# Optimization experiments

Hardware: AMD Instinct MI355X
Metric: run time of the kernel (lower is better)

## Reference

```python
import jax, jax.numpy as jnp
import numpy as np

SLOPE = 0.2  # LeakyReLU slope (DGCNN convention)

def _conv1x1(x, W, b):
    # x: [B, N, Cin], W: [Cout, Cin] -> [B, N, Cout] (Conv2d 1x1 == shared MLP)
    return jnp.einsum('bnc,oc->bno', x, W) + b

def _edgeconv(x, k, Wa, ba, Wb, bb):
    # DGCNN EdgeConv: kNN in feature space, edge MLP on (x_j - x_i, x_i), max-aggregate.
    # x: [B, N, C]
    sq = jnp.sum(x * x, axis=-1)                       # [B, N]
    inner = jnp.einsum('bnc,bmc->bnm', x, x)           # [B, N, N]
    dist = sq[:, :, None] - 2.0 * inner + sq[:, None, :]
    _, idx = jax.lax.top_k(-dist, k)                   # [B, N, k] (includes self)
    nb = jax.vmap(lambda xb, ib: xb[ib])(x, idx)       # [B, N, k, C] gather neighbors
    xi = jnp.broadcast_to(x[:, :, None, :], nb.shape)
    e = jnp.concatenate([nb - xi, xi], axis=-1)        # [B, N, k, 2C]
    h = jax.nn.leaky_relu(jnp.einsum('bnke,oe->bnko', e, Wa) + ba, SLOPE)
    h = jax.nn.leaky_relu(jnp.einsum('bnkc,oc->bnko', h, Wb) + bb, SLOPE)
    return jnp.max(h, axis=2)                          # [B, N, Cout]

def setup_inputs() -> dict:
    key = jax.random.key(0)
    ks = jax.random.split(key, 12)
    B, C, N = 2, 128, 8192
    r = 4
    out_dim = 3 * r  # 12
    def w(k, shape, fan_in):
        return (jax.random.normal(k, shape, jnp.float32) / np.sqrt(fan_in)).astype(jnp.float32)
    z = lambda n: jnp.zeros((n,), jnp.float32)
    return {
        'feature': jax.random.normal(ks[0], (B, C, N, 1), jnp.float32),
        # block 0: conv_bn_layer 128->32, EdgeConv(32->128, k=12)
        'Wc0': w(ks[1], (32, 128), 128), 'bc0': z(32),
        'We0a': w(ks[2], (128, 64), 64), 'be0a': z(128),
        'We0b': w(ks[3], (128, 128), 128), 'be0b': z(128),
        # block 1: conv_bn_layer 128->32, EdgeConv(32->128, k=4)
        'Wc1': w(ks[4], (32, 128), 128), 'bc1': z(32),
        'We1a': w(ks[5], (128, 64), 64), 'be1a': z(128),
        'We1b': w(ks[6], (128, 128), 128), 'be1b': z(128),
        # decoder: shared MLP [128 -> 6 -> 12], then Conv2d(12, 12, 1) with bias
        'Wd0': w(ks[7], (out_dim // 2, 128), 128), 'bd0': z(out_dim // 2),
        'Wd1': w(ks[8], (out_dim, out_dim // 2), out_dim // 2), 'bd1': z(out_dim),
        'Wd2': w(ks[9], (out_dim, out_dim), out_dim), 'bd2': z(out_dim),
    }

def reference(feature, Wc0, bc0, We0a, be0a, We0b, be0b,
              Wc1, bc1, We1a, be1a, We1b, be1b,
              Wd0, bd0, Wd1, bd1, Wd2, bd2):
    # feature: [B, C, N, 1] -> [B, N, C]
    x = jnp.swapaxes(jnp.squeeze(feature, -1), 1, 2)
    x = jax.nn.leaky_relu(_conv1x1(x, Wc0, bc0), SLOPE)   # 128 -> 32
    x = _edgeconv(x, 12, We0a, be0a, We0b, be0b)           # 32 -> 128, k=12
    x = jax.nn.leaky_relu(_conv1x1(x, Wc1, bc1), SLOPE)   # 128 -> 32
    x = _edgeconv(x, 4, We1a, be1a, We1b, be1b)            # 32 -> 128, k=4
    x = jax.nn.leaky_relu(_conv1x1(x, Wd0, bd0), SLOPE)   # 128 -> 6
    x = jax.nn.leaky_relu(_conv1x1(x, Wd1, bd1), SLOPE)   # 6 -> 12
    x = _conv1x1(x, Wd2, bd2)                              # final conv, no activation
    return x  # [B, N, 3*upsample_ratio] (matches squeeze(-1).permute(0,2,1))
```

## Files before the change

kernel.cpp:

```cpp
#include <hip/hip_runtime.h>

#define NPTS 8192
#define NB 2

typedef __attribute__((ext_vector_type(8))) short short8v;
typedef __attribute__((ext_vector_type(4))) float f32x4;

__device__ __forceinline__ float lrelu(float x) { return x > 0.f ? x : 0.2f * x; }
__device__ __forceinline__ float4 lrelu4(float4 a) {
    return make_float4(lrelu(a.x), lrelu(a.y), lrelu(a.z), lrelu(a.w));
}
__device__ __forceinline__ float4 fmax4(float4 a, float4 b) {
    return make_float4(fmaxf(a.x, b.x), fmaxf(a.y, b.y), fmaxf(a.z, b.z), fmaxf(a.w, b.w));
}
__device__ __forceinline__ float4 add4(float4 a, float4 b) {
    return make_float4(a.x + b.x, a.y + b.y, a.z + b.z, a.w + b.w);
}
__device__ __forceinline__ unsigned short f2bf(float f) {
    unsigned int u = __float_as_uint(f);
    return (unsigned short)((u + 0x7FFFu + ((u >> 16) & 1u)) >> 16);
}
__device__ __forceinline__ float bf2f(unsigned short h) {
    return __uint_as_float(((unsigned int)h) << 16);
}
__device__ __forceinline__ short8v scale_m2(short8v v) {
    uint4 u = *(uint4*)&v;
    u.x = (u.x + 0x00800080u) ^ 0x80008000u;
    u.y = (u.y + 0x00800080u) ^ 0x80008000u;
    u.z = (u.z + 0x00800080u) ^ 0x80008000u;
    u.w = (u.w + 0x00800080u) ^ 0x80008000u;
    return *(short8v*)&u;
}

__global__ void k_transpose_w(const float* __restrict__ Wb0, const float* __restrict__ Wb1,
                              float* __restrict__ out) {
    int t = blockIdx.x * 256 + threadIdx.x;
    if (t < 16384)      out[t] = Wb0[(t & 127) * 128 + (t >> 7)];
    else if (t < 32768) { int i = t - 16384; out[t] = Wb1[(i & 127) * 128 + (i >> 7)]; }
}

__device__ __forceinline__ void split3(float4 v, unsigned int* hp, unsigned int* mp,
                                       unsigned int* lp) {
    float c[4] = {v.x, v.y, v.z, v.w};
    unsigned short h[4], m[4], l[4];
    #pragma unroll
    for (int i = 0; i < 4; ++i) {
        h[i] = f2bf(c[i]);
        float r1 = c[i] - bf2f(h[i]);
        m[i] = f2bf(r1);
        float r2 = r1 - bf2f(m[i]);
        l[i] = f2bf(r2);
    }
    hp[0] = (unsigned int)h[0] | ((unsigned int)h[1] << 16);
    hp[1] = (unsigned int)h[2] | ((unsigned int)h[3] << 16);
    mp[0] = (unsigned int)m[0] | ((unsigned int)m[1] << 16);
    mp[1] = (unsigned int)m[2] | ((unsigned int)m[3] << 16);
    lp[0] = (unsigned int)l[0] | ((unsigned int)l[1] << 16);
    lp[1] = (unsigned int)l[2] | ((unsigned int)l[3] << 16);
}

__global__ void k_conv_in(const float* __restrict__ f, const float* __restrict__ W,
                          const float* __restrict__ bias, float* __restrict__ out,
                          float* __restrict__ sq, unsigned short* __restrict__ xh,
                          unsigned short* __restrict__ xm, unsigned short* __restrict__ xl) {
    int gid = blockIdx.x * blockDim.x + threadIdx.x;
    int b = gid >> 13, n = gid & (NPTS - 1);
    const float* fb = f + ((size_t)b << 20) + n;
    float acc[32];
    #pragma unroll
    for (int o = 0; o < 32; ++o) acc[o] = bias[o];
    #pragma unroll 4
    for (int c = 0; c < 128; ++c) {
        float xc = fb[(size_t)c * NPTS];
        #pragma unroll
        for (int o = 0; o < 32; ++o) acc[o] += xc * W[o * 128 + c];
    }
    float s = 0.f;
    float4* op = (float4*)(out + (size_t)gid * 32);
    unsigned int* hrow = (unsigned int*)(xh + (size_t)gid * 32);
    unsigned int* mrow = (unsigned int*)(xm + (size_t)gid * 32);
    unsigned int* lrow = (unsigned int*)(xl + (size_t)gid * 32);
    #pragma unroll
    for (int o4 = 0; o4 < 8; ++o4) {
        float4 v = make_float4(lrelu(acc[o4 * 4]), lrelu(acc[o4 * 4 + 1]),
                               lrelu(acc[o4 * 4 + 2]), lrelu(acc[o4 * 4 + 3]));
        s += v.x * v.x + v.y * v.y + v.z * v.z + v.w * v.w;
        op[o4] = v;
        unsigned int hp[2], mp[2], lp[2];
        split3(v, hp, mp, lp);
        *(uint2*)(hrow + o4 * 2) = make_uint2(hp[0], hp[1]);
        *(uint2*)(mrow + o4 * 2) = make_uint2(mp[0], mp[1]);
        *(uint2*)(lrow + o4 * 2) = make_uint2(lp[0], lp[1]);
    }
    sq[gid] = s;
}

__global__ __launch_bounds__(256, 2) void k_premix(const float* __restrict__ x,
                                                   const float* __restrict__ Wa,
                                                   const float* __restrict__ ba,
                                                   float* __restrict__ A,
                                                   float* __restrict__ Bm) {
    int tid = threadIdx.x;
    int q = tid >> 6;
    int p = blockIdx.x * 64 + (tid & 63);
    float4 xv[8];
    {
        const float4* xr = (const float4*)(x + (size_t)p * 32);
        #pragma unroll
        for (int u = 0; u < 8; ++u) xv[u] = xr[u];
    }
    const float* W0 = Wa + q * 32 * 64;
    float acc[32];
    #pragma unroll
    for (int o = 0; o < 32; ++o) acc[o] = 0.f;
    #pragma unroll 2
    for (int c4 = 0; c4 < 8; ++c4) {
        float4 v = xv[c4];
        #pragma unroll
        for (int o = 0; o < 32; ++o) {
            const float* w = W0 + o * 64 + c4 * 4;
            acc[o] += v.x * w[0] + v.y * w[1] + v.z * w[2] + v.w * w[3];
        }
    }
    {
        float4* op = (float4*)(A + (size_t)p * 128 + q * 32);
        #pragma unroll
        for (int o4 = 0; o4 < 8; ++o4)
            op[o4] = make_float4(acc[o4 * 4], acc[o4 * 4 + 1], acc[o4 * 4 + 2], acc[o4 * 4 + 3]);
    }
    #pragma unroll
    for (int o = 0; o < 32; ++o) acc[o] = ba[q * 32 + o];
    #pragma unroll 2
    for (int c4 = 0; c4 < 8; ++c4) {
        float4 v = xv[c4];
        #pragma unroll
        for (int o = 0; o < 32; ++o) {
            const float* w1 = W0 + o * 64 + c4 * 4;
            const float* w2 = w1 + 32;
            acc[o] += v.x * (w2[0] - w1[0]) + v.y * (w2[1] - w1[1]) +
                      v.z * (w2[2] - w1[2]) + v.w * (w2[3] - w1[3]);
        }
    }
    {
        float4* op = (float4*)(Bm + (size_t)p * 128 + q * 32);
        #pragma unroll
        for (int o4 = 0; o4 < 8; ++o4)
            op[o4] = make_float4(acc[o4 * 4], acc[o4 * 4 + 1], acc[o4 * 4 + 2], acc[o4 * 4 + 3]);
    }
}

template <int K, int JS, int C>
__global__ __launch_bounds__(128, 2) void k_knn_mfma(const unsigned short* __restrict__ xh,
                                                     const unsigned short* __restrict__ xm,
                                                     const unsigned short* __restrict__ xl,
                                                     const float* __restrict__ sqg,
                                                     float* __restrict__ cand_d,
                                                     int* __restrict__ cand_i) {
    constexpr int IT = 128;
    constexpr int JR = NPTS / JS;
    constexpr int NCH = JR / 16;
    constexpr int BPB = (NPTS / IT) * JS;
    constexpr int DS = 17;

    __shared__ float Dl[IT * DS];
    __shared__ unsigned long long bufe[C * IT];

    int tid = threadIdx.x;
    int bid = blockIdx.x;
    int b = bid / BPB;
    int r0b = bid - b * BPB;
    int itile = r0b / JS;
    int jseg = r0b - itile * JS;

    const unsigned short* xhb = xh + ((size_t)b * NPTS) * 32;
    const unsigned short* xmb = xm + ((size_t)b * NPTS) * 32;
    const unsigned short* xlb = xl + ((size_t)b * NPTS) * 32;
    const float* sqb = sqg + (size_t)b * NPTS;

    int lane = tid & 63;
    int w = tid >> 6;
    int g = lane >> 4;
    int r15 = lane & 15;

    short8v ah[4], am[4], al[4];
    #pragma unroll
    for (int t = 0; t < 4; ++t) {
        size_t ii = (size_t)(itile * IT + w * 64 + t * 16 + r15);
        ah[t] = scale_m2(*(const short8v*)(xhb + ii * 32 + g * 8));
        am[t] = scale_m2(*(const short8v*)(xmb + ii * 32 + g * 8));
        al[t] = scale_m2(*(const short8v*)(xlb + ii * 32 + g * 8));
    }
    #pragma unroll
    for (int t = 0; t < 4; ++t) {
        asm volatile("" : "+v"(ah[t]));
        asm volatile("" : "+v"(am[t]));
        asm volatile("" : "+v"(al[t]));
    }

    float bd[K]; int bi[K];
    #pragma unroll
    for (int r = 0; r < K; ++r) { bd[r] = 1e30f; bi[r] = 0; }
    float thr = 1e30f;
    int cnt = 0;

    auto flush = [&]() {
        int mc = cnt;
        #pragma unroll
        for (int off = 1; off < 64; off <<= 1) {
            int o = __shfl_xor(mc, off);
            mc = mc > o ? mc : o;
        }
        #pragma unroll 1
        for (int u = 0; u < mc; ++u) {
            unsigned long long e = bufe[u * IT + tid];
            bool valid = u < cnt;
            float dd = valid ? __uint_as_float((unsigned int)(e >> 32)) : 1e30f;
            int ji = (int)(unsigned int)e;
            #pragma unroll
            for (int r = 0; r < K; ++r) {
                bool c = dd < bd[r];
                float tf = bd[r]; int ti = bi[r];
                bd[r] = c ? dd : bd[r]; bi[r] = c ? ji : bi[r];
                dd = c ? tf : dd;       ji = c ? ti : ji;
            }
        }
        cnt = 0; thr = bd[K - 1];
    };

#define LOADBS_(J, BH, BM, BL, SV)                                             \
    do {                                                                       \
        size_t ja_ = (size_t)(J) + r15;                                        \
        BH = *(const short8v*)(xhb + ja_ * 32 + g * 8);                        \
        BM = *(const short8v*)(xmb + ja_ * 32 + g * 8);                        \
        BL = *(const short8v*)(xlb + ja_ * 32 + g * 8);                        \
        SV = sqb[(size_t)(J) + r15];                                           \
    } while (0)

#define MFMA_(BH, BM, BL, SV)                                                  \
    do {                                                                       \
        _Pragma("unroll")                                                      \
        for (int t = 0; t < 4; ++t) {                                          \
            f32x4 acc = {SV, SV, SV, SV};                                      \
            acc = __builtin_amdgcn_mfma_f32_16x16x32_bf16(am[t], BM, acc, 0, 0, 0); \
            acc = __builtin_amdgcn_mfma_f32_16x16x32_bf16(ah[t], BL, acc, 0, 0, 0); \
            acc = __builtin_amdgcn_mfma_f32_16x16x32_bf16(al[t], BH, acc, 0, 0, 0); \
            acc = __builtin_amdgcn_mfma_f32_16x16x32_bf16(ah[t], BM, acc, 0, 0, 0); \
            acc = __builtin_amdgcn_mfma_f32_16x16x32_bf16(am[t], BH, acc, 0, 0, 0); \
            acc = __builtin_amdgcn_mfma_f32_16x16x32_bf16(ah[t], BH, acc, 0, 0, 0); \
            int il_ = w * 64 + t * 16 + g * 4;                                 \
            Dl[(il_ + 0) * DS + r15] = acc[0];                                 \
            Dl[(il_ + 1) * DS + r15] = acc[1];                                 \
            Dl[(il_ + 2) * DS + r15] = acc[2];                                 \
            Dl[(il_ + 3) * DS + r15] = acc[3];                                 \
        }                                                                      \
    } while (0)

#define PACK_(D, J) ((((unsigned long long)__float_as_uint(D)) << 32) | (unsigned int)(J))

#define SELECT_(J0)                                                            \
    do {                                                                       \
        _Pragma("unroll 1")                                                    \
        for (int jq = 0; jq < 16; jq += 4) {                                   \
            float d0 = Dl[tid * DS + jq + 0];                                  \
            float d1 = Dl[tid * DS + jq + 1];                                  \
            float d2 = Dl[tid * DS + jq + 2];                                  \
            float d3 = Dl[tid * DS + jq + 3];                                  \
            int j_ = (J0) + jq;                                                \
            if (d0 < thr) { bufe[cnt * IT + tid] = PACK_(d0, j_ + 0); cnt++; } \
            if (d1 < thr) { bufe[cnt * IT + tid] = PACK_(d1, j_ + 1); cnt++; } \
            if (d2 < thr) { bufe[cnt * IT + tid] = PACK_(d2, j_ + 2); cnt++; } \
            if (d3 < thr) { bufe[cnt * IT + tid] = PACK_(d3, j_ + 3); cnt++; } \
            if (__any(cnt >= C - 3)) flush();                                  \
        }                                                                      \
    } while (0)

    int jbase = jseg * JR;
    short8v bhA, bmA, blA, bhB, bmB, blB;
    float svA, svB;
    LOADBS_(jbase, bhA, bmA, blA, svA);
    #pragma unroll 1
    for (int ch = 0; ch < NCH; ch += 2) {
        int j0 = jbase + ch * 16;
        int j1 = j0 + 16;
        LOADBS_(j1, bhB, bmB, blB, svB);
        MFMA_(bhA, bmA, blA, svA);
        SELECT_(j0);
        int j2 = (ch + 2 < NCH) ? j1 + 16 : jbase;
        LOADBS_(j2, bhA, bmA, blA, svA);
        MFMA_(bhB, bmB, blB, svB);
        SELECT_(j1);
    }
    flush();
#undef LOADBS_
#undef MFMA_
#undef PACK_
#undef SELECT_
    size_t base = ((size_t)jseg * (NB * NPTS) + (size_t)(b * NPTS) + itile * IT + tid) * K;
    #pragma unroll
    for (int r = 0; r < K; ++r) { cand_d[base + r] = bd[r]; cand_i[base + r] = bi[r]; }
}

template <int K, int JS>
__global__ __launch_bounds__(128, 4) void k_knn_merge2(const float* __restrict__ cand_d,
                                                       const int* __restrict__ cand_i,
                                                       int* __restrict__ idx_out) {
    int p = blockIdx.x * 128 + threadIdx.x;
    float bd[K]; int bi[K];
    #pragma unroll
    for (int r = 0; r < K; ++r) { bd[r] = 1e30f; bi[r] = 0; }
    float thr = 1e30f;
    #pragma unroll 1
    for (int s = 0; s < JS; ++s) {
        size_t base = ((size_t)s * (NB * NPTS) + p) * K;
        #pragma unroll 1
        for (int r = 0; r < K; ++r) {
            float d = cand_d[base + r];
            if (!(d < thr)) break;
            int j = cand_i[base + r];
            float dd = d; int ji = j;
            #pragma unroll
            for (int q = 0; q < K; ++q) {
                bool c = dd < bd[q];
                float tf = bd[q]; int ti = bi[q];
                bd[q] = c ? dd : bd[q]; bi[q] = c ? ji : bi[q];
                dd = c ? tf : dd;       ji = c ? ti : ji;
            }
            thr = bd[K - 1];
        }
    }
    int* op = idx_out + (size_t)p * K;
    #pragma unroll
    for (int r = 0; r < K; ++r) op[r] = bi[r];
}

template <int K>
__global__ __launch_bounds__(256, 1)
void k_edgeconv4(const int* __restrict__ idx,
                 const float* __restrict__ A, const float* __restrict__ Bm,
                 const float* __restrict__ WbTg, const float* __restrict__ bb,
                 float* __restrict__ y) {
    constexpr int TE = (K == 12) ? 6 : 4;
    constexpr int EPI = 16 * TE;
    constexpr int PI = EPI / K;
    constexpr int ITERS = 64 / PI;
    constexpr int NT = 256;
    constexpr int HS = 132;

    __shared__ __align__(16) float WbT[128 * 128];
    __shared__ __align__(16) float bb_s[128];
    __shared__ __align__(16) float H1[EPI * HS];
    __shared__ __align__(16) float Pm[(K == 12) ? 16 * 128 : 4];

    int tid = threadIdx.x;
    {
        const float4* sb = (const float4*)WbTg;
        float4* db = (float4*)WbT;
        #pragma unroll
        for (int i = 0; i < 16; ++i) db[tid + i * NT] = sb[tid + i * NT];
        if (tid < 128) bb_s[tid] = bb[tid];
    }

    int b = blockIdx.x >> 7;
    int pbase = (blockIdx.x & 127) * 64;
    const int* idxb = idx + ((size_t)b * NPTS) * K;
    const float4* A4 = (const float4*)(A + ((size_t)b * NPTS) * 128);
    const float4* B4 = (const float4*)(Bm + ((size_t)b * NPTS) * 128);
    float* yb = y + ((size_t)b * NPTS) * 128;

    int og = tid & 15;
    int eg = tid >> 4;
    int ebase = eg * TE;

    for (int it = 0; it < ITERS; ++it) {
        int pt0 = pbase + it * PI;
        #pragma unroll
        for (int r = 0; r < (EPI * 32) / NT; ++r) {
            int u = tid + r * NT;
            int e = u >> 5, c4 = u & 31;
            int p = pt0 + e / K;
            int j = idxb[(size_t)p * K + (e % K)];
            float4 av = A4[(size_t)j * 32 + c4];
            float4 bv = B4[(size_t)p * 32 + c4];
            *(float4*)&H1[e * HS + 4 * c4] = lrelu4(add4(av, bv));
        }
        __syncthreads();
        float4 acc[TE][2];
        {
            float4 blo = *(const float4*)&bb_s[og * 8];
            float4 bhi = *(const float4*)&bb_s[og * 8 + 4];
            #pragma unroll
            for (int e = 0; e < TE; ++e) { acc[e][0] = blo; acc[e][1] = bhi; }
        }
        #pragma unroll 2
        for (int c4 = 0; c4 < 32; ++c4) {
            float4 hv[TE];
            #pragma unroll
            for (int e = 0; e < TE; ++e)
                hv[e] = *(const float4*)&H1[(ebase + e) * HS + 4 * c4];
            #pragma unroll
            for (int j = 0; j < 4; ++j) {
                const float* wr = &WbT[(4 * c4 + j) * 128 + og * 8];
                float4 wlo = *(const float4*)wr;
                float4 whi = *(const float4*)(wr + 4);
                #pragma unroll
                for (int e = 0; e < TE; ++e) {
                    float hc = (j == 0) ? hv[e].x : (j == 1) ? hv[e].y : (j == 2) ? hv[e].z : hv[e].w;
                    acc[e][0].x += hc * wlo.x; acc[e][0].y += hc * wlo.y;
                    acc[e][0].z += hc * wlo.z; acc[e][0].w += hc * wlo.w;
                    acc[e][1].x += hc * whi.x; acc[e][1].y += hc * whi.y;
                    acc[e][1].z += hc * whi.z; acc[e][1].w += hc * whi.w;
                }
            }
        }
        float4 mlo = lrelu4(acc[0][0]), mhi = lrelu4(acc[0][1]);
        #pragma unroll
        for (int e = 1; e < TE; ++e) {
            mlo = fmax4(mlo, lrelu4(acc[e][0]));
            mhi = fmax4(mhi, lrelu4(acc[e][1]));
        }
        if constexpr (K == 4) {
            float4* yp = (float4*)&yb[((size_t)(pt0 + eg)) * 128 + og * 8];
            yp[0] = mlo; yp[1] = mhi;
            __syncthreads();
        } else {
            *(float4*)&Pm[eg * 128 + og * 8] = mlo;
            *(float4*)&Pm[eg * 128 + og * 8 + 4] = mhi;
            __syncthreads();
            #pragma unroll
            for (int r = 0; r < 4; ++r) {
                int u = tid + r * NT;
                int p = u >> 7, o = u & 127;
                yb[((size_t)(pt0 + p)) * 128 + o] =
                    fmaxf(Pm[(2 * p) * 128 + o], Pm[(2 * p + 1) * 128 + o]);
            }
        }
    }
}

__global__ void k_conv_mid(const float* __restrict__ xin, const float* __restrict__ W,
                           const float* __restrict__ bias, float* __restrict__ out,
                           float* __restrict__ sq, unsigned short* __restrict__ xh,
                           unsigned short* __restrict__ xm, unsigned short* __restrict__ xl) {
    int gid = blockIdx.x * blockDim.x + threadIdx.x;
    const float4* row = (const float4*)(xin + (size_t)gid * 128);
    float acc[32];
    #pragma unroll
    for (int o = 0; o < 32; ++o) acc[o] = bias[o];
    #pragma unroll 2
    for (int c4 = 0; c4 < 32; ++c4) {
        float4 v = row[c4];
        #pragma unroll
        for (int o = 0; o < 32; ++o) {
            const float* w = W + o * 128 + c4 * 4;
            acc[o] += v.x * w[0] + v.y * w[1] + v.z * w[2] + v.w * w[3];
        }
    }
    float s = 0.f;
    float4* op = (float4*)(out + (size_t)gid * 32);
    unsigned int* hrow = (unsigned int*)(xh + (size_t)gid * 32);
    unsigned int* mrow = (unsigned int*)(xm + (size_t)gid * 32);
    unsigned int* lrow = (unsigned int*)(xl + (size_t)gid * 32);
    #pragma unroll
    for (int o4 = 0; o4 < 8; ++o4) {
        float4 v = make_float4(lrelu(acc[o4 * 4]), lrelu(acc[o4 * 4 + 1]),
                               lrelu(acc[o4 * 4 + 2]), lrelu(acc[o4 * 4 + 3]));
        s += v.x * v.x + v.y * v.y + v.z * v.z + v.w * v.w;
        op[o4] = v;
        unsigned int hp[2], mp[2], lp[2];
        split3(v, hp, mp, lp);
        *(uint2*)(hrow + o4 * 2) = make_uint2(hp[0], hp[1]);
        *(uint2*)(mrow + o4 * 2) = make_uint2(mp[0], mp[1]);
        *(uint2*)(lrow + o4 * 2) = make_uint2(lp[0], lp[1]);
    }
    sq[gid] = s;
}

__global__ void k_decoder(const float* __restrict__ xin,
                          const float* __restrict__ W0, const float* __restrict__ b0,
                          const float* __restrict__ W1, const float* __restrict__ b1,
                          const float* __restrict__ W2, const float* __restrict__ b2,
                          float* __restrict__ out) {
    int gid = blockIdx.x * blockDim.x + threadIdx.x;
    const float4* row = (const float4*)(xin + (size_t)gid * 128);
    float h0[6];
    #pragma unroll
    for (int o = 0; o < 6; ++o) h0[o] = b0[o];
    #pragma unroll 4
    for (int c4 = 0; c4 < 32; ++c4) {
        float4 v = row[c4];
        #pragma unroll
        for (int o = 0; o < 6; ++o) {
            const float* w = W0 + o * 128 + c4 * 4;
            h0[o] += v.x * w[0] + v.y * w[1] + v.z * w[2] + v.w * w[3];
        }
    }
    #pragma unroll
    for (int o = 0; o < 6; ++o) h0[o] = lrelu(h0[o]);
    float h1[12];
    #pragma unroll
    for (int o = 0; o < 12; ++o) {
        float a = b1[o];
        #pragma unroll
        for (int j = 0; j < 6; ++j) a += W1[o * 6 + j] * h0[j];
        h1[o] = lrelu(a);
    }
    float* op = out + (size_t)gid * 12;
    #pragma unroll
    for (int o = 0; o < 12; ++o) {
        float a = b2[o];
        #pragma unroll
        for (int j = 0; j < 12; ++j) a += W2[o * 12 + j] * h1[j];
        op[o] = a;
    }
}

extern "C" void kernel_launch(void* const* d_in, const int* in_sizes, int n_in,
                              void* d_out, int out_size, void* d_ws, size_t ws_size,
                              hipStream_t stream) {
    const float* feature = (const float*)d_in[0];
    const float* Wc0 = (const float*)d_in[1];
    const float* bc0 = (const float*)d_in[2];
    const float* We0a = (const float*)d_in[3];
    const float* be0a = (const float*)d_in[4];
    const float* We0b = (const float*)d_in[5];
    const float* be0b = (const float*)d_in[6];
    const float* Wc1 = (const float*)d_in[7];
    const float* bc1 = (const float*)d_in[8];
    const float* We1a = (const float*)d_in[9];
    const float* be1a = (const float*)d_in[10];
    const float* We1b = (const float*)d_in[11];
    const float* be1b = (const float*)d_in[12];
    const float* Wd0 = (const float*)d_in[13];
    const float* bd0 = (const float*)d_in[14];
    const float* Wd1 = (const float*)d_in[15];
    const float* bd1 = (const float*)d_in[16];
    const float* Wd2 = (const float*)d_in[17];
    const float* bd2 = (const float*)d_in[18];
    float* out = (float*)d_out;

    float* f = (float*)d_ws;
    float* x0   = f;
    float* x1   = f + 524288;
    int*   idx0 = (int*)(f + 1048576);
    int*   idx1 = (int*)(f + 1245184);
    float* wT   = f + 1310720;
    float* Zab  = f + 1343488;
    float* Abuf = Zab;
    float* Bbuf = Zab + 2097152;
    float* Y    = f + 5537792;
    float* sq0  = f + 7634944;
    float* sq1  = f + 7651328;
    unsigned short* xh0 = (unsigned short*)(f + 524288);
    unsigned short* xm0 = (unsigned short*)(f + 786432);
    unsigned short* xl0 = (unsigned short*)(f + 1048576);
    float* c0d  = f + 1343488;
    int*   c0i  = (int*)(f + 4489216);
    unsigned short* xh1 = (unsigned short*)Zab;
    unsigned short* xm1 = (unsigned short*)(Zab + 262144);
    unsigned short* xl1 = (unsigned short*)(Zab + 524288);
    float* c1d  = Zab + 786432;
    int*   c1i  = (int*)(Zab + 1835008);
    float* WbT0 = wT;
    float* WbT1 = wT + 16384;

    k_transpose_w<<<128, 256, 0, stream>>>(We0b, We1b, wT);
    k_conv_in<<<64, 256, 0, stream>>>(feature, Wc0, bc0, x0, sq0, xh0, xm0, xl0);
    k_knn_mfma<12, 16, 10><<<2048, 128, 0, stream>>>(xh0, xm0, xl0, sq0, c0d, c0i);
    k_knn_merge2<12, 16><<<128, 128, 0, stream>>>(c0d, c0i, idx0);
    k_premix<<<256, 256, 0, stream>>>(x0, We0a, be0a, Abuf, Bbuf);
    k_edgeconv4<12><<<256, 256, 0, stream>>>(idx0, Abuf, Bbuf, WbT0, be0b, Y);
    k_conv_mid<<<64, 256, 0, stream>>>(Y, Wc1, bc1, x1, sq1, xh1, xm1, xl1);
    k_knn_mfma<4, 16, 8><<<2048, 128, 0, stream>>>(xh1, xm1, xl1, sq1, c1d, c1i);
    k_knn_merge2<4, 16><<<128, 128, 0, stream>>>(c1d, c1i, idx1);
    k_premix<<<256, 256, 0, stream>>>(x1, We1a, be1a, Abuf, Bbuf);
    k_edgeconv4<4><<<256, 256, 0, stream>>>(idx1, Abuf, Bbuf, WbT1, be1b, Y);
    k_decoder<<<64, 256, 0, stream>>>(Y, Wd0, bd0, Wd1, bd1, Wd2, bd2, out);
}
```

Measured before the change: 623.6 us.

## Move EdgeConv second layer onto bf16 MFMA with split-precision weights

Replaces the scalar FP32 second-layer GEMM of the edge MLP with bf16 MFMA 16x16x32, using a hi/lo split of both activations and weights (three MFMAs per tile) to keep close to FP32 accuracy. Weights are prepacked once into MFMA fragment layout in a new prepack kernel and staged into LDS. The max over neighbours is done in registers with lane shuffles instead of through an LDS staging buffer. The launch changes to 512 blocks of 128 threads. The split-bf16 product drops the lo*lo term, which adds a small accuracy risk.

```diff
diff --git a/kernel.cpp b/kernel.cpp
--- a/kernel.cpp
+++ b/kernel.cpp
@@ -9,12 +9,6 @@
 __device__ __forceinline__ float lrelu(float x) { return x > 0.f ? x : 0.2f * x; }
 __device__ __forceinline__ float4 lrelu4(float4 a) {
     return make_float4(lrelu(a.x), lrelu(a.y), lrelu(a.z), lrelu(a.w));
-}
-__device__ __forceinline__ float4 fmax4(float4 a, float4 b) {
-    return make_float4(fmaxf(a.x, b.x), fmaxf(a.y, b.y), fmaxf(a.z, b.z), fmaxf(a.w, b.w));
-}
-__device__ __forceinline__ float4 add4(float4 a, float4 b) {
-    return make_float4(a.x + b.x, a.y + b.y, a.z + b.z, a.w + b.w);
 }
 __device__ __forceinline__ unsigned short f2bf(float f) {
     unsigned int u = __float_as_uint(f);
@@ -32,13 +26,6 @@
     return *(short8v*)&u;
 }
 
-__global__ void k_transpose_w(const float* __restrict__ Wb0, const float* __restrict__ Wb1,
-                              float* __restrict__ out) {
-    int t = blockIdx.x * 256 + threadIdx.x;
-    if (t < 16384)      out[t] = Wb0[(t & 127) * 128 + (t >> 7)];
-    else if (t < 32768) { int i = t - 16384; out[t] = Wb1[(i & 127) * 128 + (i >> 7)]; }
-}
-
 __device__ __forceinline__ void split3(float4 v, unsigned int* hp, unsigned int* mp,
                                        unsigned int* lp) {
     float c[4] = {v.x, v.y, v.z, v.w};
@@ -57,6 +44,25 @@
     mp[1] = (unsigned int)m[2] | ((unsigned int)m[3] << 16);
     lp[0] = (unsigned int)l[0] | ((unsigned int)l[1] << 16);
     lp[1] = (unsigned int)l[2] | ((unsigned int)l[3] << 16);
+}
+
+__global__ void k_prepack_wb(const float* __restrict__ Wb0, const float* __restrict__ Wb1,
+                             unsigned short* __restrict__ out) {
+    int t = blockIdx.x * 256 + threadIdx.x;
+    int L = t >> 14;
+    int idx = t & 16383;
+    int frag = idx >> 9;
+    int lane = (idx >> 3) & 63;
+    int e = idx & 7;
+    int kc = frag >> 3, nt = frag & 7;
+    int k = kc * 32 + (lane >> 4) * 8 + e;
+    int n = nt * 16 + (lane & 15);
+    const float* Wb = L ? Wb1 : Wb0;
+    float val = Wb[n * 128 + k];
+    unsigned short hi = f2bf(val);
+    unsigned short lo = f2bf(val - bf2f(hi));
+    out[(L * 2 + 0) * 16384 + idx] = hi;
+    out[(L * 2 + 1) * 16384 + idx] = lo;
 }
 
 __global__ void k_conv_in(const float* __restrict__ f, const float* __restrict__ W,
@@ -334,104 +340,112 @@
 }
 
 template <int K>
-__global__ __launch_bounds__(256, 1)
-void k_edgeconv4(const int* __restrict__ idx,
+__global__ __launch_bounds__(128, 2)
+void k_edgeconv5(const int* __restrict__ idx,
                  const float* __restrict__ A, const float* __restrict__ Bm,
-                 const float* __restrict__ WbTg, const float* __restrict__ bb,
+                 const unsigned short* __restrict__ wpackL,
+                 const float* __restrict__ bb,
                  float* __restrict__ y) {
-    constexpr int TE = (K == 12) ? 6 : 4;
-    constexpr int EPI = 16 * TE;
-    constexpr int PI = EPI / K;
-    constexpr int ITERS = 64 / PI;
-    constexpr int NT = 256;
-    constexpr int HS = 132;
-
-    __shared__ __align__(16) float WbT[128 * 128];
-    __shared__ __align__(16) float bb_s[128];
-    __shared__ __align__(16) float H1[EPI * HS];
-    __shared__ __align__(16) float Pm[(K == 12) ? 16 * 128 : 4];
+    __shared__ __align__(16) unsigned short Wfr[32768];
+    __shared__ float bb_s[128];
 
     int tid = threadIdx.x;
     {
-        const float4* sb = (const float4*)WbTg;
-        float4* db = (float4*)WbT;
-        #pragma unroll
-        for (int i = 0; i < 16; ++i) db[tid + i * NT] = sb[tid + i * NT];
+        const uint4* src = (const uint4*)wpackL;
+        uint4* dst = (uint4*)Wfr;
+        #pragma unroll
+        for (int i = 0; i < 32; ++i) dst[tid + i * 128] = src[tid + i * 128];
         if (tid < 128) bb_s[tid] = bb[tid];
     }
-
-    int b = blockIdx.x >> 7;
-    int pbase = (blockIdx.x & 127) * 64;
+    __syncthreads();
+
+    int lane = tid & 63;
+    int wv = tid >> 6;
+    int e = lane & 15;
+    int q = lane >> 4;
+    int b = blockIdx.x >> 8;
     const int* idxb = idx + ((size_t)b * NPTS) * K;
     const float4* A4 = (const float4*)(A + ((size_t)b * NPTS) * 128);
     const float4* B4 = (const float4*)(Bm + ((size_t)b * NPTS) * 128);
     float* yb = y + ((size_t)b * NPTS) * 128;
 
-    int og = tid & 15;
-    int eg = tid >> 4;
-    int ebase = eg * TE;
-
-    for (int it = 0; it < ITERS; ++it) {
-        int pt0 = pbase + it * PI;
-        #pragma unroll
-        for (int r = 0; r < (EPI * 32) / NT; ++r) {
-            int u = tid + r * NT;
-            int e = u >> 5, c4 = u & 31;
-            int p = pt0 + e / K;
-            int j = idxb[(size_t)p * K + (e % K)];
-            float4 av = A4[(size_t)j * 32 + c4];
-            float4 bv = B4[(size_t)p * 32 + c4];
-            *(float4*)&H1[e * HS + 4 * c4] = lrelu4(add4(av, bv));
-        }
-        __syncthreads();
-        float4 acc[TE][2];
-        {
-            float4 blo = *(const float4*)&bb_s[og * 8];
-            float4 bhi = *(const float4*)&bb_s[og * 8 + 4];
+    float bbv[8];
+    #pragma unroll
+    for (int nt = 0; nt < 8; ++nt) bbv[nt] = bb_s[nt * 16 + e];
+
+    constexpr int TILES = (K == 12) ? 16 : 4;
+    int base0 = (blockIdx.x & 255) * ((K == 12) ? 32 : 32);
+
+    #pragma unroll 1
+    for (int ti = 0; ti < TILES; ++ti) {
+        int prow, j;
+        int ptile = 0;
+        if constexpr (K == 12) {
+            prow = base0 + wv * 16 + ti;
+            int eidx = (e < 12) ? e : 0;
+            j = idxb[prow * 12 + eidx];
+        } else {
+            ptile = (base0 >> 2) + wv * 4 + ti;
+            prow = ptile * 4 + (e >> 2);
+            j = idxb[prow * 4 + (e & 3)];
+        }
+        short8v ahh[4], ahl[4];
+        #pragma unroll
+        for (int kc = 0; kc < 4; ++kc) {
+            int c4off = kc * 8 + q * 2;
+            float4 a0 = A4[(size_t)j * 32 + c4off];
+            float4 a1 = A4[(size_t)j * 32 + c4off + 1];
+            float4 b0 = B4[(size_t)prow * 32 + c4off];
+            float4 b1 = B4[(size_t)prow * 32 + c4off + 1];
+            float h[8];
+            h[0] = lrelu(a0.x + b0.x); h[1] = lrelu(a0.y + b0.y);
+            h[2] = lrelu(a0.z + b0.z); h[3] = lrelu(a0.w + b0.w);
+            h[4] = lrelu(a1.x + b1.x); h[5] = lrelu(a1.y + b1.y);
+            h[6] = lrelu(a1.z + b1.z); h[7] = lrelu(a1.w + b1.w);
+            unsigned int wh[4], wl[4];
             #pragma unroll
-            for (int e = 0; e < TE; ++e) { acc[e][0] = blo; acc[e][1] = bhi; }
-        }
-        #pragma unroll 2
-        for (int c4 = 0; c4 < 32; ++c4) {
-            float4 hv[TE];
+            for (int i2 = 0; i2 < 4; ++i2) {
+                unsigned short h0 = f2bf(h[2 * i2]);
+                unsigned short h1b = f2bf(h[2 * i2 + 1]);
+                unsigned short l0 = f2bf(h[2 * i2] - bf2f(h0));
+                unsigned short l1 = f2bf(h[2 * i2 + 1] - bf2f(h1b));
+                wh[i2] = (unsigned int)h0 | ((unsigned int)h1b << 16);
+                wl[i2] = (unsigned int)l0 | ((unsigned int)l1 << 16);
+            }
+            uint4 uh = make_uint4(wh[0], wh[1], wh[2], wh[3]);
+            uint4 ul = make_uint4(wl[0], wl[1], wl[2], wl[3]);
+            ahh[kc] = *(short8v*)&uh;
+            ahl[kc] = *(short8v*)&ul;
+        }
+        f32x4 acc[8];
+        #pragma unroll
+        for (int nt = 0; nt < 8; ++nt) {
+            f32x4 ai = {bbv[nt], bbv[nt], bbv[nt], bbv[nt]};
+            acc[nt] = ai;
+        }
+        #pragma unroll
+        for (int kc = 0; kc < 4; ++kc) {
             #pragma unroll
-            for (int e = 0; e < TE; ++e)
-                hv[e] = *(const float4*)&H1[(ebase + e) * HS + 4 * c4];
-            #pragma unroll
-            for (int j = 0; j < 4; ++j) {
-                const float* wr = &WbT[(4 * c4 + j) * 128 + og * 8];
-                float4 wlo = *(const float4*)wr;
-                float4 whi = *(const float4*)(wr + 4);
-                #pragma unroll
-                for (int e = 0; e < TE; ++e) {
-                    float hc = (j == 0) ? hv[e].x : (j == 1) ? hv[e].y : (j == 2) ? hv[e].z : hv[e].w;
-                    acc[e][0].x += hc * wlo.x; acc[e][0].y += hc * wlo.y;
-                    acc[e][0].z += hc * wlo.z; acc[e][0].w += hc * wlo.w;
-                    acc[e][1].x += hc * whi.x; acc[e][1].y += hc * whi.y;
-                    acc[e][1].z += hc * whi.z; acc[e][1].w += hc * whi.w;
-                }
+            for (int nt = 0; nt < 8; ++nt) {
+                short8v bh = *(const short8v*)&Wfr[(kc * 8 + nt) * 512 + lane * 8];
+                short8v bl = *(const short8v*)&Wfr[16384 + (kc * 8 + nt) * 512 + lane * 8];
+                acc[nt] = __builtin_amdgcn_mfma_f32_16x16x32_bf16(ahh[kc], bh, acc[nt], 0, 0, 0);
+                acc[nt] = __builtin_amdgcn_mfma_f32_16x16x32_bf16(ahh[kc], bl, acc[nt], 0, 0, 0);
+                acc[nt] = __builtin_amdgcn_mfma_f32_16x16x32_bf16(ahl[kc], bh, acc[nt], 0, 0, 0);
             }
         }
-        float4 mlo = lrelu4(acc[0][0]), mhi = lrelu4(acc[0][1]);
-        #pragma unroll
-        for (int e = 1; e < TE; ++e) {
-            mlo = fmax4(mlo, lrelu4(acc[e][0]));
-            mhi = fmax4(mhi, lrelu4(acc[e][1]));
-        }
-        if constexpr (K == 4) {
-            float4* yp = (float4*)&yb[((size_t)(pt0 + eg)) * 128 + og * 8];
-            yp[0] = mlo; yp[1] = mhi;
-            __syncthreads();
-        } else {
-            *(float4*)&Pm[eg * 128 + og * 8] = mlo;
-            *(float4*)&Pm[eg * 128 + og * 8 + 4] = mhi;
-            __syncthreads();
-            #pragma unroll
-            for (int r = 0; r < 4; ++r) {
-                int u = tid + r * NT;
-                int p = u >> 7, o = u & 127;
-                yb[((size_t)(pt0 + p)) * 128 + o] =
-                    fmaxf(Pm[(2 * p) * 128 + o], Pm[(2 * p + 1) * 128 + o]);
+        #pragma unroll
+        for (int nt = 0; nt < 8; ++nt) {
+            float m = lrelu(acc[nt][0]);
+            m = fmaxf(m, lrelu(acc[nt][1]));
+            m = fmaxf(m, lrelu(acc[nt][2]));
+            m = fmaxf(m, lrelu(acc[nt][3]));
+            if constexpr (K == 12) {
+                m = fmaxf(m, __shfl_xor(m, 16));
+                m = fmaxf(m, __shfl_xor(m, 32));
+                if (lane < 16) yb[(size_t)prow * 128 + nt * 16 + lane] = m;
+            } else {
+                yb[(size_t)(ptile * 4 + q) * 128 + nt * 16 + e] = m;
             }
         }
     }
@@ -543,7 +557,7 @@
     float* x1   = f + 524288;
     int*   idx0 = (int*)(f + 1048576);
     int*   idx1 = (int*)(f + 1245184);
-    float* wT   = f + 1310720;
+    unsigned short* wpack = (unsigned short*)(f + 1310720);
     float* Zab  = f + 1343488;
     float* Abuf = Zab;
     float* Bbuf = Zab + 2097152;
@@ -560,19 +574,17 @@
     unsigned short* xl1 = (unsigned short*)(Zab + 524288);
     float* c1d  = Zab + 786432;
     int*   c1i  = (int*)(Zab + 1835008);
-    float* WbT0 = wT;
-    float* WbT1 = wT + 16384;
-
-    k_transpose_w<<<128, 256, 0, stream>>>(We0b, We1b, wT);
+
+    k_prepack_wb<<<128, 256, 0, stream>>>(We0b, We1b, wpack);
     k_conv_in<<<64, 256, 0, stream>>>(feature, Wc0, bc0, x0, sq0, xh0, xm0, xl0);
     k_knn_mfma<12, 16, 10><<<2048, 128, 0, stream>>>(xh0, xm0, xl0, sq0, c0d, c0i);
     k_knn_merge2<12, 16><<<128, 128, 0, stream>>>(c0d, c0i, idx0);
     k_premix<<<256, 256, 0, stream>>>(x0, We0a, be0a, Abuf, Bbuf);
-    k_edgeconv4<12><<<256, 256, 0, stream>>>(idx0, Abuf, Bbuf, WbT0, be0b, Y);
+    k_edgeconv5<12><<<512, 128, 0, stream>>>(idx0, Abuf, Bbuf, wpack, be0b, Y);
     k_conv_mid<<<64, 256, 0, stream>>>(Y, Wc1, bc1, x1, sq1, xh1, xm1, xl1);
     k_knn_mfma<4, 16, 8><<<2048, 128, 0, stream>>>(xh1, xm1, xl1, sq1, c1d, c1i);
     k_knn_merge2<4, 16><<<128, 128, 0, stream>>>(c1d, c1i, idx1);
     k_premix<<<256, 256, 0, stream>>>(x1, We1a, be1a, Abuf, Bbuf);
-    k_edgeconv4<4><<<256, 256, 0, stream>>>(idx1, Abuf, Bbuf, WbT1, be1b, Y);
+    k_edgeconv5<4><<<512, 128, 0, stream>>>(idx1, Abuf, Bbuf, wpack + 32768, be1b, Y);
     k_decoder<<<64, 256, 0, stream>>>(Y, Wd0, bd0, Wd1, bd1, Wd2, bd2, out);
 }
```

After: 584.1 us. 1.07x faster.
